# Performance work log

Hardware: AMD Instinct MI355X
Metric: run time of the kernel (lower is better)

Reference implementation:

```python
import jax, jax.numpy as jnp
import numpy as np

N_NODES = 646  # fixed by nn.LayerNorm([646, 64])
LN_EPS = 1e-5


def gcn_conv(x, edge_index, W, b):
    """PyG GCNConv: out = D^-1/2 (A+I) D^-1/2 (x W) + b, scatter-add at target."""
    n = x.shape[0]
    h = x @ W  # [N, out_dim]
    loop = jnp.arange(n, dtype=edge_index.dtype)
    row = jnp.concatenate([edge_index[0], loop])  # source
    col = jnp.concatenate([edge_index[1], loop])  # target
    deg = jax.ops.segment_sum(jnp.ones_like(col, dtype=h.dtype), col, num_segments=n)
    dinv = jnp.where(deg > 0, jax.lax.rsqrt(deg), 0.0)
    norm = dinv[row] * dinv[col]  # [E+N]
    out = jax.ops.segment_sum(h[row] * norm[:, None], col, num_segments=n)
    return out + b


def setup_inputs() -> dict:
    key = jax.random.key(0)
    ks = jax.random.split(key, 8)
    F, H, L, E = 32768, 64, 128, 646 * 64
    x = jax.random.normal(ks[0], (N_NODES, F), dtype=jnp.float32)
    edge_index = jax.random.randint(ks[1], (2, E), 0, N_NODES, dtype=jnp.int64)
    s = 1.0 / np.sqrt(F)
    W1 = jax.random.normal(ks[2], (F, H), dtype=jnp.float32) * s
    b1 = jax.random.normal(ks[3], (H,), dtype=jnp.float32) * 0.01
    W2 = jax.random.normal(ks[4], (H, L), dtype=jnp.float32) * (1.0 / np.sqrt(H))
    b2 = jax.random.normal(ks[5], (L,), dtype=jnp.float32) * 0.01
    LPw = jax.random.normal(ks[6], (F, H), dtype=jnp.float32) * s
    LPb = jax.random.normal(ks[7], (H,), dtype=jnp.float32) * 0.01
    return {"x": x, "edge_index": edge_index, "W1": W1, "b1": b1,
            "W2": W2, "b2": b2, "LPw": LPw, "LPb": LPb}


def reference(x, edge_index, W1, b1, W2, b2, LPw, LPb):
    res = x @ LPw + LPb                       # Linear residual branch [N, 64]
    h = gcn_conv(x, edge_index, W1, b1)       # GCN1 [N, 64]
    h = res + h
    h = h * jax.nn.sigmoid(h)                 # SiLU
    # LayerNorm over BOTH dims [646, 64], no affine (elementwise_affine=False)
    mu = jnp.mean(h)
    var = jnp.mean(jnp.square(h - mu))
    h = (h - mu) * jax.lax.rsqrt(var + LN_EPS)
    out = gcn_conv(h, edge_index, W2, b2)     # GCN2 [N, num_label]
    return out
```

## Files before the change

### kernel.cpp

```cpp
#include <hip/hip_runtime.h>
#include <hip/hip_bf16.h>

#define NN 646
#define FF 32768
#define HH 64
#define LL 128
#define TOT (NN*HH)
#define OUTTOT (NN*LL)
#define WT_STRIDE (FF + 32)
#define KSPLIT 64
#define KSLICE (FF / KSPLIT)
#define BK 32
#define NSTEP (KSLICE / BK)
#define NMT 6
#define NGEMM (NMT * KSPLIT)

typedef float f32x4 __attribute__((ext_vector_type(4)));
typedef short short8 __attribute__((ext_vector_type(8)));

__device__ __forceinline__ unsigned short f2bf(float f) {
  __hip_bfloat16 h = __float2bfloat16(f);
  return __builtin_bit_cast(unsigned short, h);
}
__device__ __forceinline__ short8 pack8(float4 u, float4 v) {
  short8 r;
  r[0] = (short)f2bf(u.x); r[1] = (short)f2bf(u.y);
  r[2] = (short)f2bf(u.z); r[3] = (short)f2bf(u.w);
  r[4] = (short)f2bf(v.x); r[5] = (short)f2bf(v.y);
  r[6] = (short)f2bf(v.z); r[7] = (short)f2bf(v.w);
  return r;
}
__device__ __forceinline__ void gload16(const void* g, void* l) {
  __builtin_amdgcn_global_load_lds(
      (const __attribute__((address_space(1))) void*)g,
      (__attribute__((address_space(3))) void*)l, 16, 0, 0);
}
__device__ __forceinline__ bool probe_i64(const int* e32, int* orr) {
  if (threadIdx.x == 0) *orr = 0;
  __syncthreads();
  if (threadIdx.x < 256 && e32[2 * threadIdx.x + 1] != 0) atomicOr(orr, 1);
  __syncthreads();
  return *orr == 0;
}

__global__ __launch_bounds__(256) void k_init(const float* __restrict__ W1,
                                              const float* __restrict__ LPw,
                                              unsigned short* __restrict__ wt,
                                              const int* __restrict__ e32, int E,
                                              int* __restrict__ cntp,
                                              const float* __restrict__ W2,
                                              float* __restrict__ cs,
                                              float* __restrict__ stats) {
  if (blockIdx.x < 512) {
    __shared__ float t[64][129];
    int k0 = blockIdx.x * 64;
    for (int idx = threadIdx.x; idx < 64 * 128; idx += 256) {
      int kk = idx >> 7, n = idx & 127;
      float v = (n < 64) ? W1[(size_t)(k0 + kk) * 64 + n]
                         : LPw[(size_t)(k0 + kk) * 64 + (n - 64)];
      t[kk][n] = v;
    }
    __syncthreads();
    for (int idx = threadIdx.x; idx < 1024; idx += 256) {
      int n = idx >> 3;
      int kc = (idx & 7) * 8;
      short8 v;
#pragma unroll
      for (int u = 0; u < 8; ++u) v[u] = (short)f2bf(t[kc + u][n]);
      *reinterpret_cast<short8*>(&wt[(size_t)n * WT_STRIDE + k0 + kc]) = v;
    }
    return;
  }
  if (blockIdx.x == 576) {
    __shared__ float r2[2][128];
    int j = threadIdx.x & 127, h = threadIdx.x >> 7;
    if (threadIdx.x < 2) stats[threadIdx.x] = 0.f;
    float a = 0.f;
    for (int k = h * 32; k < h * 32 + 32; ++k) a += W2[k * LL + j];
    r2[h][j] = a;
    __syncthreads();
    if (h == 0) cs[j] = r2[0][j] + r2[1][j];
    return;
  }
  __shared__ int lcnt[648];
  __shared__ int orr;
  int hb = blockIdx.x - 512;
  for (int i = threadIdx.x; i < 648; i += 256) lcnt[i] = 0;
  bool i64 = probe_i64(e32, &orr);
  const int* cp = i64 ? (e32 + 2 * (size_t)E) : (e32 + E);
  int st = i64 ? 2 : 1;
  for (int e = hb * 256 + threadIdx.x; e < E; e += 64 * 256)
    atomicAdd(&lcnt[cp[(size_t)e * st]], 1);
  __syncthreads();
  for (int i = threadIdx.x; i < 648; i += 256) cntp[hb * 648 + i] = lcnt[i];
}

__global__ __launch_bounds__(256, 2) void k_gemm(const float* __restrict__ x,
                                                 const unsigned short* __restrict__ wt,
                                                 float* __restrict__ partial,
                                                 const int* __restrict__ cntp, int E,
                                                 int* __restrict__ offsets,
                                                 float* __restrict__ dinv,
                                                 int* __restrict__ cursor) {
  __shared__ __align__(16) float As[3][128 * BK];
  __shared__ __align__(16) unsigned short Bs[3][128 * BK];

  int p = blockIdx.x;
  if (p == NGEMM) {
    __shared__ int wtot[4];
    int tid = threadIdx.x;
    int b = 3 * tid;
    int c0 = 0, c1 = 0, c2 = 0;
    if (b < NN) {
#pragma unroll 8
      for (int h = 0; h < 64; ++h) {
        c0 += cntp[h * 648 + b];
        c1 += (b + 1 < NN) ? cntp[h * 648 + b + 1] : 0;
        c2 += (b + 2 < NN) ? cntp[h * 648 + b + 2] : 0;
      }
    }
    int s = c0 + c1 + c2;
    int lane = tid & 63, wv = tid >> 6;
    int run = s;
#pragma unroll
    for (int o = 1; o < 64; o <<= 1) { int v = __shfl_up(run, o); if (lane >= o) run += v; }
    if (lane == 63) wtot[wv] = run;
    __syncthreads();
    int wbase = 0;
    for (int i = 0; i < wv; ++i) wbase += wtot[i];
    int excl = wbase + run - s;
    if (b < NN)     { offsets[b]     = excl;           cursor[b]     = excl;           dinv[b]     = rsqrtf((float)(c0 + 1)); }
    if (b + 1 < NN) { offsets[b + 1] = excl + c0;      cursor[b + 1] = excl + c0;      dinv[b + 1] = rsqrtf((float)(c1 + 1)); }
    if (b + 2 < NN) { offsets[b + 2] = excl + c0 + c1; cursor[b + 2] = excl + c0 + c1; dinv[b + 2] = rsqrtf((float)(c2 + 1)); }
    if (tid == 0) offsets[NN] = E;
    return;
  }

  int xcd = p & 7, idx = p >> 3;
  int ks = xcd + 8 * (idx / NMT);
  int mt = idx % NMT;
  int tid = threadIdx.x;
  int w = tid >> 6, l = tid & 63;
  int lr = l & 15, g = l >> 4;
  int wr = w * 32;
  int ksbase = ks * KSLICE;

  f32x4 z = {0.f, 0.f, 0.f, 0.f};
  f32x4 a00 = z, a01 = z, a02 = z, a03 = z, a04 = z, a05 = z, a06 = z, a07 = z;
  f32x4 a10 = z, a11 = z, a12 = z, a13 = z, a14 = z, a15 = z, a16 = z, a17 = z;

  auto STAGE = [&](int buf, int step) {
    int kb = ksbase + step * BK;
#pragma unroll
    for (int j = 0; j < 4; ++j) {
      int pp = j * 256 + tid;
      int row = pp >> 3, cc = pp & 7;
      int c = cc ^ (row & 7);
      int rowg = mt * 128 + row; if (rowg > NN - 1) rowg = NN - 1;
      gload16(x + (size_t)rowg * FF + kb + c * 4, (char*)(&As[buf][0]) + pp * 16);
    }
#pragma unroll
    for (int j = 0; j < 2; ++j) {
      int pp = j * 256 + tid;
      int row = pp >> 2, cc = pp & 3;
      int c = cc ^ (row & 3);
      gload16(wt + (size_t)row * WT_STRIDE + kb + c * 8,
              (char*)(&Bs[buf][0]) + pp * 16);
    }
  };

  auto COMPUTE = [&](int buf) {
    const char* Ab = (const char*)(&As[buf][0]);
    const char* Bb = (const char*)(&Bs[buf][0]);
    short8 af0, af1;
    {
      int row = wr + lr, rm = row & 7;
      float4 lo = *(const float4*)(Ab + (row * 8 + ((g * 2) ^ rm)) * 16);
      float4 hi = *(const float4*)(Ab + (row * 8 + ((g * 2 + 1) ^ rm)) * 16);
      af0 = pack8(lo, hi);
    }
    {
      int row = wr + 16 + lr, rm = row & 7;
      float4 lo = *(const float4*)(Ab + (row * 8 + ((g * 2) ^ rm)) * 16);
      float4 hi = *(const float4*)(Ab + (row * 8 + ((g * 2 + 1) ^ rm)) * 16);
      af1 = pack8(lo, hi);
    }
#define DO_NF(NF, A0, A1)                                                        \
    {                                                                            \
      int brow = NF * 16 + lr;                                                   \
      short8 bv = *(const short8*)(Bb + (brow * 4 + (g ^ (brow & 3))) * 16);     \
      A0 = __builtin_amdgcn_mfma_f32_16x16x32_bf16(af0, bv, A0, 0, 0, 0);        \
      A1 = __builtin_amdgcn_mfma_f32_16x16x32_bf16(af1, bv, A1, 0, 0, 0);        \
    }
    DO_NF(0, a00, a10) DO_NF(1, a01, a11) DO_NF(2, a02, a12) DO_NF(3, a03, a13)
    DO_NF(4, a04, a14) DO_NF(5, a05, a15) DO_NF(6, a06, a16) DO_NF(7, a07, a17)
#undef DO_NF
  };

  STAGE(0, 0);
  STAGE(1, 1);
#pragma unroll
  for (int t = 0; t < NSTEP; ++t) {
    if (t + 1 < NSTEP) {
      asm volatile("s_waitcnt vmcnt(6)" ::: "memory");
    } else {
      asm volatile("s_waitcnt vmcnt(0)" ::: "memory");
    }
    __builtin_amdgcn_s_barrier();
    if (t + 2 < NSTEP) STAGE((t + 2) % 3, t + 2);
    COMPUTE(t % 3);
  }

  float* pp = partial + (size_t)ks * OUTTOT;
#define EPI(MF, NF, ACC)                                                         \
  {                                                                              \
    _Pragma("unroll")                                                            \
    for (int j = 0; j < 4; ++j) {                                                \
      int m = mt * 128 + wr + MF * 16 + g * 4 + j;                               \
      if (m < NN) pp[m * LL + NF * 16 + lr] = ACC[j];                            \
    }                                                                            \
  }
  EPI(0, 0, a00) EPI(0, 1, a01) EPI(0, 2, a02) EPI(0, 3, a03)
  EPI(0, 4, a04) EPI(0, 5, a05) EPI(0, 6, a06) EPI(0, 7, a07)
  EPI(1, 0, a10) EPI(1, 1, a11) EPI(1, 2, a12) EPI(1, 3, a13)
  EPI(1, 4, a14) EPI(1, 5, a15) EPI(1, 6, a16) EPI(1, 7, a17)
#undef EPI
}

__global__ __launch_bounds__(256) void k_redplace(const float* __restrict__ partial,
                                                  const float* __restrict__ LPb,
                                                  float* __restrict__ hcat,
                                                  const int* __restrict__ e32, int E,
                                                  int* __restrict__ cursor,
                                                  int* __restrict__ srcs) {
  if (blockIdx.x < 81) {
    int i4 = blockIdx.x * 256 + threadIdx.x;
    if (i4 * 4 >= OUTTOT) return;
    f32x4 s = {0.f, 0.f, 0.f, 0.f};
#pragma unroll 8
    for (int ks = 0; ks < KSPLIT; ++ks)
      s += *reinterpret_cast<const f32x4*>(partial + (size_t)ks * OUTTOT + i4 * 4);
    int n = (i4 * 4) & 127;
    if (n & 64) s += *reinterpret_cast<const f32x4*>(LPb + (n - 64));
    *reinterpret_cast<f32x4*>(hcat + i4 * 4) = s;
    return;
  }
  __shared__ int orr;
  bool i64 = probe_i64(e32, &orr);
  int e = (blockIdx.x - 81) * 256 + threadIdx.x;
  if (e >= E) return;
  const int* rp = e32;
  const int* cp = i64 ? (e32 + 2 * (size_t)E) : (e32 + E);
  int st = i64 ? 2 : 1;
  int r = rp[(size_t)e * st];
  int c = cp[(size_t)e * st];
  int pos = atomicAdd(&cursor[c], 1);
  srcs[pos] = r;
}

__global__ __launch_bounds__(256) void k_fuse1(const int* __restrict__ offs,
                                               const int* __restrict__ srcs,
                                               const float* __restrict__ dinv,
                                               const float* __restrict__ hcat,
                                               const float* __restrict__ b1,
                                               const float* __restrict__ W2,
                                               float* __restrict__ hwr,
                                               float* __restrict__ sdi,
                                               float* __restrict__ stats) {
  int c = blockIdx.x;
  int j = threadIdx.x & 63, qt = threadIdx.x >> 6;
  int o0 = offs[c], o1 = offs[c + 1];
  float acc = 0.f, sd = 0.f;
  for (int i = o0 + qt; i < o1; i += 4) {
    int r = srcs[i];
    float dr = dinv[r];
    acc += hcat[r * LL + j] * dr;
    sd += dr;
  }
  __shared__ float red[4][64];
  __shared__ float sdl[4];
  __shared__ float hnl[64];
  red[qt][j] = acc;
  if (j == 0) sdl[qt] = sd;
  __syncthreads();
  if (qt == 0) {
    float di = dinv[c];
    float gb = (red[0][j] + red[1][j] + red[2][j] + red[3][j]) * di;
    float t = hcat[c * LL + 64 + j] + b1[j] + gb + hcat[c * LL + j] * di * di;
    float s = t / (1.f + __expf(-t));
    hnl[j] = s;
    float sum = s, sq = s * s;
#pragma unroll
    for (int o = 32; o; o >>= 1) { sum += __shfl_down(sum, o); sq += __shfl_down(sq, o); }
    if (j == 0) {
      atomicAdd(&stats[0], sum);
      atomicAdd(&stats[1], sq);
      sdi[c] = sdl[0] + sdl[1] + sdl[2] + sdl[3] + di;
    }
  }
  __syncthreads();
  int j2 = threadIdx.x & 127, h = threadIdx.x >> 7;
  float a2 = 0.f;
#pragma unroll
  for (int k = h * 32; k < h * 32 + 32; ++k) a2 += hnl[k] * W2[k * LL + j2];
  __shared__ float r2[2][128];
  r2[h][j2] = a2;
  __syncthreads();
  if (h == 0) hwr[c * LL + j2] = (r2[0][j2] + r2[1][j2]) * dinv[c];
}

__global__ __launch_bounds__(256) void k_fuse2(const int* __restrict__ offs,
                                               const int* __restrict__ srcs,
                                               const float* __restrict__ dinv,
                                               const float* __restrict__ hwr,
                                               const float* __restrict__ b2,
                                               const float* __restrict__ cs,
                                               const float* __restrict__ sdi,
                                               const float* __restrict__ stats,
                                               float* __restrict__ out) {
  int c = blockIdx.x;
  int j = threadIdx.x & 127, hf = threadIdx.x >> 7;
  int o0 = offs[c], o1 = offs[c + 1];
  float acc = 0.f;
  for (int i = o0 + hf; i < o1; i += 2) acc += hwr[srcs[i] * LL + j];
  __shared__ float red[2][128];
  red[hf][j] = acc;
  __syncthreads();
  if (hf == 0) {
    float mu = stats[0] * (1.f / TOT);
    float var = stats[1] * (1.f / TOT) - mu * mu;
    float rs = rsqrtf(var + 1e-5f);
    float S = red[0][j] + red[1][j] + hwr[c * LL + j];
    out[c * LL + j] = b2[j] + dinv[c] * (rs * S - rs * mu * cs[j] * sdi[c]);
  }
}

extern "C" void kernel_launch(void* const* d_in, const int* in_sizes, int n_in,
                              void* d_out, int out_size, void* d_ws, size_t ws_size,
                              hipStream_t stream) {
  const float* x   = (const float*)d_in[0];
  const int*   e32 = (const int*)d_in[1];
  const float* W1  = (const float*)d_in[2];
  const float* b1  = (const float*)d_in[3];
  const float* W2  = (const float*)d_in[4];
  const float* b2  = (const float*)d_in[5];
  const float* LPw = (const float*)d_in[6];
  const float* LPb = (const float*)d_in[7];
  int E = in_sizes[1] / 2;
  float* out = (float*)d_out;

  char* ws = (char*)d_ws;
  size_t o_wt      = 0;
  size_t o_partial = 8396800;
  size_t o_hcat    = o_partial + (size_t)KSPLIT * OUTTOT * 4;
  size_t o_hwr     = o_hcat + 330752;
  size_t o_dinv    = o_hwr + 330752;
  size_t o_offs    = o_dinv + 2816;
  size_t o_cntp    = o_offs + 2816;
  size_t o_stat    = o_cntp + 165888;
  size_t o_cur     = o_stat + 256;
  size_t o_srcs    = o_cur + 2816;
  size_t o_cs      = o_srcs + 165376;
  size_t o_sdi     = o_cs + 512;

  unsigned short* wt = (unsigned short*)(ws + o_wt);
  float* partial = (float*)(ws + o_partial);
  float* hcat    = (float*)(ws + o_hcat);
  float* hwr     = (float*)(ws + o_hwr);
  float* dinv    = (float*)(ws + o_dinv);
  int*   offs    = (int*)(ws + o_offs);
  int*   cntp    = (int*)(ws + o_cntp);
  float* stats   = (float*)(ws + o_stat);
  int*   cursor  = (int*)(ws + o_cur);
  int*   srcs    = (int*)(ws + o_srcs);
  float* cs      = (float*)(ws + o_cs);
  float* sdi     = (float*)(ws + o_sdi);

  k_init<<<577, 256, 0, stream>>>(W1, LPw, wt, e32, E, cntp, W2, cs, stats);
  k_gemm<<<NGEMM + 1, 256, 0, stream>>>(x, wt, partial, cntp, E, offs, dinv, cursor);
  k_redplace<<<243, 256, 0, stream>>>(partial, LPb, hcat, e32, E, cursor, srcs);
  k_fuse1<<<NN, 256, 0, stream>>>(offs, srcs, dinv, hcat, b1, W2, hwr, sdi, stats);
  k_fuse2<<<NN, 256, 0, stream>>>(offs, srcs, dinv, hwr, b2, cs, sdi, stats, out);
}
```

Measured before the change: 80.76 us.

## Merge post-GEMM kernels into one cooperative kernel with grid syncs

Replaces the three post-GEMM launches (reduce/scatter, fuse1, fuse2) with a single cooperative kernel of 646 blocks that separates the phases with grid-wide syncs. The aim is to remove two kernel launch gaps and their drain/fill overhead. In exchange it adds the cost of grid barriers and depends on all 646 blocks being co-resident for the cooperative launch to work.

```diff
diff --git a/kernel.cpp b/kernel.cpp
--- a/kernel.cpp
+++ b/kernel.cpp
@@ -1,5 +1,8 @@
 #include <hip/hip_runtime.h>
 #include <hip/hip_bf16.h>
+#include <hip/hip_cooperative_groups.h>
+
+namespace cg = cooperative_groups;
 
 #define NN 646
 #define FF 32768
@@ -227,111 +230,112 @@
 #undef EPI
 }
 
-__global__ __launch_bounds__(256) void k_redplace(const float* __restrict__ partial,
-                                                  const float* __restrict__ LPb,
-                                                  float* __restrict__ hcat,
-                                                  const int* __restrict__ e32, int E,
-                                                  int* __restrict__ cursor,
-                                                  int* __restrict__ srcs) {
-  if (blockIdx.x < 81) {
-    int i4 = blockIdx.x * 256 + threadIdx.x;
-    if (i4 * 4 >= OUTTOT) return;
-    f32x4 s = {0.f, 0.f, 0.f, 0.f};
-#pragma unroll 8
-    for (int ks = 0; ks < KSPLIT; ++ks)
-      s += *reinterpret_cast<const f32x4*>(partial + (size_t)ks * OUTTOT + i4 * 4);
-    int n = (i4 * 4) & 127;
-    if (n & 64) s += *reinterpret_cast<const f32x4*>(LPb + (n - 64));
-    *reinterpret_cast<f32x4*>(hcat + i4 * 4) = s;
-    return;
-  }
+__global__ __launch_bounds__(256) void k_post(const float* __restrict__ partial,
+                                              const float* __restrict__ LPb,
+                                              float* __restrict__ hcat,
+                                              const int* __restrict__ e32, int E,
+                                              int* __restrict__ cursor,
+                                              int* __restrict__ srcs,
+                                              const int* __restrict__ offs,
+                                              const float* __restrict__ dinv,
+                                              const float* __restrict__ b1,
+                                              const float* __restrict__ W2,
+                                              float* __restrict__ hwr,
+                                              float* __restrict__ sdi,
+                                              float* __restrict__ stats,
+                                              const float* __restrict__ b2,
+                                              const float* __restrict__ cs,
+                                              float* __restrict__ out) {
+  cg::grid_group gg = cg::this_grid();
+  int bid = blockIdx.x, tid = threadIdx.x;
   __shared__ int orr;
-  bool i64 = probe_i64(e32, &orr);
-  int e = (blockIdx.x - 81) * 256 + threadIdx.x;
-  if (e >= E) return;
-  const int* rp = e32;
-  const int* cp = i64 ? (e32 + 2 * (size_t)E) : (e32 + E);
-  int st = i64 ? 2 : 1;
-  int r = rp[(size_t)e * st];
-  int c = cp[(size_t)e * st];
-  int pos = atomicAdd(&cursor[c], 1);
-  srcs[pos] = r;
-}
-
-__global__ __launch_bounds__(256) void k_fuse1(const int* __restrict__ offs,
-                                               const int* __restrict__ srcs,
-                                               const float* __restrict__ dinv,
-                                               const float* __restrict__ hcat,
-                                               const float* __restrict__ b1,
-                                               const float* __restrict__ W2,
-                                               float* __restrict__ hwr,
-                                               float* __restrict__ sdi,
-                                               float* __restrict__ stats) {
-  int c = blockIdx.x;
-  int j = threadIdx.x & 63, qt = threadIdx.x >> 6;
-  int o0 = offs[c], o1 = offs[c + 1];
-  float acc = 0.f, sd = 0.f;
-  for (int i = o0 + qt; i < o1; i += 4) {
-    int r = srcs[i];
-    float dr = dinv[r];
-    acc += hcat[r * LL + j] * dr;
-    sd += dr;
-  }
   __shared__ float red[4][64];
   __shared__ float sdl[4];
   __shared__ float hnl[64];
-  red[qt][j] = acc;
-  if (j == 0) sdl[qt] = sd;
-  __syncthreads();
-  if (qt == 0) {
-    float di = dinv[c];
-    float gb = (red[0][j] + red[1][j] + red[2][j] + red[3][j]) * di;
-    float t = hcat[c * LL + 64 + j] + b1[j] + gb + hcat[c * LL + j] * di * di;
-    float s = t / (1.f + __expf(-t));
-    hnl[j] = s;
-    float sum = s, sq = s * s;
-#pragma unroll
-    for (int o = 32; o; o >>= 1) { sum += __shfl_down(sum, o); sq += __shfl_down(sq, o); }
-    if (j == 0) {
-      atomicAdd(&stats[0], sum);
-      atomicAdd(&stats[1], sq);
-      sdi[c] = sdl[0] + sdl[1] + sdl[2] + sdl[3] + di;
-    }
-  }
-  __syncthreads();
-  int j2 = threadIdx.x & 127, h = threadIdx.x >> 7;
-  float a2 = 0.f;
-#pragma unroll
-  for (int k = h * 32; k < h * 32 + 32; ++k) a2 += hnl[k] * W2[k * LL + j2];
   __shared__ float r2[2][128];
-  r2[h][j2] = a2;
-  __syncthreads();
-  if (h == 0) hwr[c * LL + j2] = (r2[0][j2] + r2[1][j2]) * dinv[c];
-}
-
-__global__ __launch_bounds__(256) void k_fuse2(const int* __restrict__ offs,
-                                               const int* __restrict__ srcs,
-                                               const float* __restrict__ dinv,
-                                               const float* __restrict__ hwr,
-                                               const float* __restrict__ b2,
-                                               const float* __restrict__ cs,
-                                               const float* __restrict__ sdi,
-                                               const float* __restrict__ stats,
-                                               float* __restrict__ out) {
-  int c = blockIdx.x;
-  int j = threadIdx.x & 127, hf = threadIdx.x >> 7;
-  int o0 = offs[c], o1 = offs[c + 1];
-  float acc = 0.f;
-  for (int i = o0 + hf; i < o1; i += 2) acc += hwr[srcs[i] * LL + j];
-  __shared__ float red[2][128];
-  red[hf][j] = acc;
-  __syncthreads();
-  if (hf == 0) {
-    float mu = stats[0] * (1.f / TOT);
-    float var = stats[1] * (1.f / TOT) - mu * mu;
-    float rs = rsqrtf(var + 1e-5f);
-    float S = red[0][j] + red[1][j] + hwr[c * LL + j];
-    out[c * LL + j] = b2[j] + dinv[c] * (rs * S - rs * mu * cs[j] * sdi[c]);
+
+  if (bid < 81) {
+    int i4 = bid * 256 + tid;
+    if (i4 * 4 < OUTTOT) {
+      f32x4 s = {0.f, 0.f, 0.f, 0.f};
+#pragma unroll 8
+      for (int ks = 0; ks < KSPLIT; ++ks)
+        s += *reinterpret_cast<const f32x4*>(partial + (size_t)ks * OUTTOT + i4 * 4);
+      int n = (i4 * 4) & 127;
+      if (n & 64) s += *reinterpret_cast<const f32x4*>(LPb + (n - 64));
+      *reinterpret_cast<f32x4*>(hcat + i4 * 4) = s;
+    }
+  } else if (bid < 243) {
+    bool i64 = probe_i64(e32, &orr);
+    int e = (bid - 81) * 256 + tid;
+    if (e < E) {
+      const int* rp = e32;
+      const int* cp = i64 ? (e32 + 2 * (size_t)E) : (e32 + E);
+      int st = i64 ? 2 : 1;
+      int r = rp[(size_t)e * st];
+      int c = cp[(size_t)e * st];
+      int pos = atomicAdd(&cursor[c], 1);
+      srcs[pos] = r;
+    }
+  }
+  gg.sync();
+
+  {
+    int c = bid;
+    int j = tid & 63, qt = tid >> 6;
+    int o0 = offs[c], o1 = offs[c + 1];
+    float acc = 0.f, sd = 0.f;
+    for (int i = o0 + qt; i < o1; i += 4) {
+      int r = srcs[i];
+      float dr = dinv[r];
+      acc += hcat[r * LL + j] * dr;
+      sd += dr;
+    }
+    red[qt][j] = acc;
+    if (j == 0) sdl[qt] = sd;
+    __syncthreads();
+    if (qt == 0) {
+      float di = dinv[c];
+      float gb = (red[0][j] + red[1][j] + red[2][j] + red[3][j]) * di;
+      float t = hcat[c * LL + 64 + j] + b1[j] + gb + hcat[c * LL + j] * di * di;
+      float s = t / (1.f + __expf(-t));
+      hnl[j] = s;
+      float sum = s, sq = s * s;
+#pragma unroll
+      for (int o = 32; o; o >>= 1) { sum += __shfl_down(sum, o); sq += __shfl_down(sq, o); }
+      if (j == 0) {
+        atomicAdd(&stats[0], sum);
+        atomicAdd(&stats[1], sq);
+        sdi[c] = sdl[0] + sdl[1] + sdl[2] + sdl[3] + di;
+      }
+    }
+    __syncthreads();
+    int j2 = tid & 127, h = tid >> 7;
+    float a2 = 0.f;
+#pragma unroll
+    for (int k = h * 32; k < h * 32 + 32; ++k) a2 += hnl[k] * W2[k * LL + j2];
+    r2[h][j2] = a2;
+    __syncthreads();
+    if (h == 0) hwr[c * LL + j2] = (r2[0][j2] + r2[1][j2]) * dinv[c];
+  }
+  gg.sync();
+
+  {
+    int c = bid;
+    int j = tid & 127, hf = tid >> 7;
+    int o0 = offs[c], o1 = offs[c + 1];
+    float acc = 0.f;
+    for (int i = o0 + hf; i < o1; i += 2) acc += hwr[srcs[i] * LL + j];
+    __syncthreads();
+    r2[hf][j] = acc;
+    __syncthreads();
+    if (hf == 0) {
+      float mu = stats[0] * (1.f / TOT);
+      float var = stats[1] * (1.f / TOT) - mu * mu;
+      float rs = rsqrtf(var + 1e-5f);
+      float S = r2[0][j] + r2[1][j] + hwr[c * LL + j];
+      out[c * LL + j] = b2[j] + dinv[c] * (rs * S - rs * mu * cs[j] * sdi[c]);
+    }
   }
 }
 
@@ -378,7 +382,8 @@
 
   k_init<<<577, 256, 0, stream>>>(W1, LPw, wt, e32, E, cntp, W2, cs, stats);
   k_gemm<<<NGEMM + 1, 256, 0, stream>>>(x, wt, partial, cntp, E, offs, dinv, cursor);
-  k_redplace<<<243, 256, 0, stream>>>(partial, LPb, hcat, e32, E, cursor, srcs);
-  k_fuse1<<<NN, 256, 0, stream>>>(offs, srcs, dinv, hcat, b1, W2, hwr, sdi, stats);
-  k_fuse2<<<NN, 256, 0, stream>>>(offs, srcs, dinv, hwr, b2, cs, sdi, stats, out);
-}
+
+  void* args[] = {&partial, &LPb, &hcat, &e32, &E, &cursor, &srcs, &offs, &dinv,
+                  &b1, &W2, &hwr, &sdi, &stats, &b2, &cs, &out};
+  hipLaunchCooperativeKernel((void*)k_post, dim3(NN), dim3(256), args, 0, stream);
+}
```

Measured after the change: 223.8 us. 177% more time.
